# Kernel tuning notes

Measured on AMD Instinct MI355X. Metric: run time of the kernel, lower is better.

Reference implementation:

```python
import jax, jax.numpy as jnp
import numpy as np

POSE_IDS = np.array([0, 4, 8, 12, 16])
BN_EPS = 1e-5


def setup_inputs() -> dict:
    key = jax.random.key(0)
    ks = jax.random.split(key, 8)
    N, C, H, W = 64, 2048, 24, 12
    P, Cl = 5, 256
    Cm = C + P * Cl  # 3328
    return {
        "x": jax.random.normal(ks[0], (N, C, H, W), jnp.float32),
        "poses": jax.random.uniform(ks[1], (N, 17, 4), jnp.float32),
        "local_w": jax.random.normal(ks[2], (P, Cl, C), jnp.float32) * 0.02,
        "local_b": jnp.zeros((P, Cl), jnp.float32),
        "local_gamma": jnp.ones((P, Cl), jnp.float32),
        "local_beta": jnp.zeros((P, Cl), jnp.float32),
        "local_mean": jax.random.normal(ks[3], (P, Cl), jnp.float32) * 0.1,
        "local_var": jax.random.uniform(ks[4], (P, Cl), jnp.float32, 0.5, 1.5),
        "merge_w": jax.random.normal(ks[5], (C, Cm), jnp.float32) * 0.02,
        "merge_b": jnp.zeros((C,), jnp.float32),
        "merge_gamma": jnp.ones((C,), jnp.float32),
        "merge_beta": jnp.zeros((C,), jnp.float32),
        "merge_mean": jax.random.normal(ks[6], (C,), jnp.float32) * 0.1,
        "merge_var": jax.random.uniform(ks[7], (C,), jnp.float32, 0.5, 1.5),
    }


def reference(x, poses, local_w, local_b, local_gamma, local_beta, local_mean,
              local_var, merge_w, merge_b, merge_gamma, merge_beta, merge_mean,
              merge_var):
    N, C, H, W = x.shape
    kp = poses[:, jnp.asarray(POSE_IDS), :]  # [N,P,4]
    # box = [left, top, w, h]; clamp to [0, 0.75]; scale whole box by confidence
    half = jnp.full_like(kp[..., 0], 0.5)
    box = jnp.stack([kp[..., 0] - 0.25, kp[..., 1] - 0.25, half, half], axis=-1)
    box = jnp.clip(box, 0.0, 0.75) * kp[..., 2:3]
    # integer ROI bounds on the feature grid (round-half-to-even like torch)
    xs = jnp.maximum(0, jnp.round(W * box[..., 0])).astype(jnp.int32)          # [N,P]
    xe = jnp.minimum(W - 1, jnp.round(W * (box[..., 0] + box[..., 2]))).astype(jnp.int32)
    ys = jnp.maximum(0, jnp.round(H * box[..., 1])).astype(jnp.int32)
    ye = jnp.minimum(H - 1, jnp.round(H * (box[..., 1] + box[..., 3]))).astype(jnp.int32)
    rows = jnp.arange(H)
    cols = jnp.arange(W)
    mh = (rows[None, None, :] >= ys[..., None]) & (rows[None, None, :] < ye[..., None])  # [N,P,H]
    mw = (cols[None, None, :] >= xs[..., None]) & (cols[None, None, :] < xe[..., None])  # [N,P,W]
    mask = (mh[..., :, None] & mw[..., None, :]).astype(x.dtype)  # [N,P,H,W]
    # masked average pool over the ROI (single pass over x)
    sums = jnp.einsum('nchw,nphw->npc', x, mask)
    area = ((ye - ys) * (xe - xs)).astype(x.dtype)
    avg = sums / jnp.where(area > 0, area, 1.0)[..., None]  # [N,P,C], 0 for empty ROIs
    # per-part 1x1 conv + BN(eval) + ReLU -> [N,P,Cl]
    loc = jnp.einsum('npc,pkc->npk', avg, local_w) + local_b[None]
    loc = (loc - local_mean[None]) * (local_gamma[None] / jnp.sqrt(local_var[None] + BN_EPS)) + local_beta[None]
    loc = jax.nn.relu(loc)
    # global max pool -> [N,C]
    gfeat = x.max(axis=(2, 3))
    cat = jnp.concatenate([loc.reshape(N, -1), gfeat], axis=1)  # [N, P*Cl + C]
    # merge 1x1 conv + BN(eval) + ReLU
    y = cat @ merge_w.T + merge_b
    y = (y - merge_mean) * (merge_gamma / jnp.sqrt(merge_var + BN_EPS)) + merge_beta
    y = jax.nn.relu(y)
    # F.normalize(p=2, dim=1)
    norm = jnp.linalg.norm(y, axis=1, keepdims=True)
    return y / jnp.maximum(norm, 1e-12)
```

## Files before the change

### kernel.cpp

```cpp
#include <hip/hip_runtime.h>

#define N_   64
#define C_   2048
#define HW_  288
#define P_   5
#define CM_  3328
#define LOC_ 1280
#define SEGC 8
#define SEGM 13

#define PITCH 28

__global__ __launch_bounds__(256) void kB(const float* __restrict__ x,
    const float* __restrict__ poses,
    float* __restrict__ avg, float* __restrict__ cat) {
  __shared__ float lds[2][256 * PITCH];
  const int t  = threadIdx.x;
  const int n  = blockIdx.x >> 3;
  const int cb = (blockIdx.x & 7) << 8;
  const int chbase = n * C_ + cb;

  unsigned MH[P_], MW[P_];
  float INV[P_];
  const float* kpn = poses + (size_t)n * 68;
#pragma unroll
  for (int p = 0; p < P_; ++p) {
    const float* kp = kpn + 16 * p;
    float px = kp[0], py = kp[1], z = kp[2];
    float bx = fminf(fmaxf(px - 0.25f, 0.f), 0.75f) * z;
    float by = fminf(fmaxf(py - 0.25f, 0.f), 0.75f) * z;
    float bw = 0.5f * z;
    float bh = 0.5f * z;
    int xs = (int)fmaxf(0.f,  rintf(12.f * bx));
    int xe = (int)fminf(11.f, rintf(12.f * (bx + bw)));
    int ys = (int)fmaxf(0.f,  rintf(24.f * by));
    int ye = (int)fminf(23.f, rintf(24.f * (by + bh)));
    MH[p] = ((1u << ye) - 1u) & ~((1u << ys) - 1u);
    MW[p] = ((1u << xe) - 1u) & ~((1u << xs) - 1u);
    int area = (ye - ys) * (xe - xs);
    INV[p] = area > 0 ? 1.f / (float)area : 1.f;
  }

  const float4* x4 = (const float4*)x;
  size_t gbase[6];
  int    loff[6];
#pragma unroll
  for (int k = 0; k < 6; ++k) {
    unsigned flat = k * 256 + t;
    unsigned cl = flat / 6u;
    unsigned j  = flat - 6u * cl;
    gbase[k] = (size_t)(chbase + cl) * 72 + j;
    loff[k]  = cl * PITCH + 4 * j;
  }

  float4 rg[6];
  auto loadRegs = [&](int ci) {
#pragma unroll
    for (int k = 0; k < 6; ++k) rg[k] = x4[gbase[k] + ci * 6];
  };
  auto writeRegs = [&](int db) {
#pragma unroll
    for (int k = 0; k < 6; ++k) *(float4*)&lds[db][loff[k]] = rg[k];
  };

  float s[P_] = {0.f, 0.f, 0.f, 0.f, 0.f};
  float mx = -3.402823466e+38f;

  loadRegs(0);
  writeRegs(0);
  __syncthreads();
  for (int ci = 0; ci < 12; ++ci) {
    if (ci + 1 < 12) loadRegs(ci + 1);
    const float* row = &lds[ci & 1][t * PITCH];
#pragma unroll
    for (int r = 0; r < 2; ++r) {
      int h = 2 * ci + r;
      float4 a = *(const float4*)(row + r * 12 + 0);
      float4 b = *(const float4*)(row + r * 12 + 4);
      float4 c = *(const float4*)(row + r * 12 + 8);
      float m1 = fmaxf(fmaxf(a.x, a.y), fmaxf(a.z, a.w));
      float m2 = fmaxf(fmaxf(b.x, b.y), fmaxf(b.z, b.w));
      float m3 = fmaxf(fmaxf(c.x, c.y), fmaxf(c.z, c.w));
      mx = fmaxf(mx, fmaxf(m1, fmaxf(m2, m3)));
#pragma unroll
      for (int p = 0; p < P_; ++p) {
        unsigned cm = ((MH[p] >> h) & 1u) ? MW[p] : 0u;
        if (cm) {
          float t0 = ((cm & 0x001u) ? a.x : 0.f) + ((cm & 0x002u) ? a.y : 0.f);
          float t1 = ((cm & 0x004u) ? a.z : 0.f) + ((cm & 0x008u) ? a.w : 0.f);
          float t2 = ((cm & 0x010u) ? b.x : 0.f) + ((cm & 0x020u) ? b.y : 0.f);
          float t3 = ((cm & 0x040u) ? b.z : 0.f) + ((cm & 0x080u) ? b.w : 0.f);
          float t4 = ((cm & 0x100u) ? c.x : 0.f) + ((cm & 0x200u) ? c.y : 0.f);
          float t5 = ((cm & 0x400u) ? c.z : 0.f) + ((cm & 0x800u) ? c.w : 0.f);
          s[p] += ((t0 + t1) + (t2 + t3)) + (t4 + t5);
        }
      }
    }
    if (ci + 1 < 12) {
      writeRegs((ci + 1) & 1);
      __syncthreads();
    }
  }

  int c = cb + t;
  cat[(size_t)n * CM_ + LOC_ + c] = mx;
#pragma unroll
  for (int p = 0; p < P_; ++p)
    avg[((size_t)n * P_ + p) * C_ + c] = s[p] * INV[p];
}

template<int GSEG>
__device__ __forceinline__ void gemm_tile(const float* __restrict__ Ag, int lda,
                                          const float* __restrict__ Wg, int ldw,
                                          float* __restrict__ Og, int ldo,
                                          float* As, float* Ws) {
  const int t  = threadIdx.x;
  const int nq = t & 15;
  const int kq = t >> 4;
  const int c4 = (t & 15) << 2;
  const int rr = t >> 4;
  float acc[4][4] = {};
  for (int g = 0; g < GSEG; ++g) {
    __syncthreads();
#pragma unroll
    for (int i = 0; i < 4; ++i) {
      int r = rr + (i << 4);
      *(float4*)&As[r * 68 + c4] = *(const float4*)&Ag[(size_t)r * lda + (g << 6) + c4];
      *(float4*)&Ws[r * 68 + c4] = *(const float4*)&Wg[(size_t)r * ldw + (g << 6) + c4];
    }
    __syncthreads();
#pragma unroll
    for (int c = 0; c < 64; c += 4) {
      float4 a[4], w[4];
#pragma unroll
      for (int i = 0; i < 4; ++i) a[i] = *(const float4*)&As[(nq + (i << 4)) * 68 + c];
#pragma unroll
      for (int j = 0; j < 4; ++j) w[j] = *(const float4*)&Ws[(kq + (j << 4)) * 68 + c];
#pragma unroll
      for (int i = 0; i < 4; ++i)
#pragma unroll
        for (int j = 0; j < 4; ++j)
          acc[i][j] += a[i].x * w[j].x + a[i].y * w[j].y + a[i].z * w[j].z + a[i].w * w[j].w;
    }
  }
#pragma unroll
  for (int i = 0; i < 4; ++i)
#pragma unroll
    for (int j = 0; j < 4; ++j)
      Og[(size_t)(nq + (i << 4)) * ldo + kq + (j << 4)] = acc[i][j];
}

__global__ __launch_bounds__(256) void kC(const float* __restrict__ avg,
                                          const float* __restrict__ local_w,
                                          float* __restrict__ locP) {
  __shared__ float As[64 * 68];
  __shared__ float Ws[64 * 68];
  int b  = blockIdx.x;
  int tl = b >> 3;
  int sg = b & 7;
  int p  = tl >> 2;
  int kt = tl & 3;
  const float* Ag = avg + p * C_ + (sg << 8);
  const float* Wg = local_w + ((size_t)p * 256 + (kt << 6)) * C_ + (sg << 8);
  float* Og = locP + (size_t)sg * (N_ * LOC_) + (p << 8) + (kt << 6);
  gemm_tile<4>(Ag, P_ * C_, Wg, C_, Og, LOC_, As, Ws);
}

__global__ __launch_bounds__(256) void kC2(const float* __restrict__ locP,
    const float* __restrict__ lb, const float* __restrict__ lg, const float* __restrict__ lbe,
    const float* __restrict__ lm, const float* __restrict__ lv,
    float* __restrict__ cat) {
  int i = blockIdx.x * 256 + threadIdx.x;
  int n = i / LOC_;
  int q = i - n * LOC_;
  float s = 0.f;
#pragma unroll
  for (int sg = 0; sg < SEGC; ++sg) s += locP[(size_t)sg * (N_ * LOC_) + i];
  float sc = lg[q] / sqrtf(lv[q] + 1e-5f);
  float v = (s + lb[q] - lm[q]) * sc + lbe[q];
  cat[(size_t)n * CM_ + q] = fmaxf(v, 0.f);
}

__global__ __launch_bounds__(256) void kD(const float* __restrict__ cat,
                                          const float* __restrict__ merge_w,
                                          float* __restrict__ mrgP) {
  __shared__ float As[64 * 68];
  __shared__ float Ws[64 * 68];
  int b  = blockIdx.x;
  int jt = b / SEGM;
  int sg = b - jt * SEGM;
  const float* Ag = cat + (sg << 8);
  const float* Wg = merge_w + (size_t)(jt << 6) * CM_ + (sg << 8);
  float* Og = mrgP + (size_t)sg * (N_ * C_) + (jt << 6);
  gemm_tile<4>(Ag, CM_, Wg, CM_, Og, C_, As, Ws);
}

__global__ __launch_bounds__(256) void kE(const float* __restrict__ mrgP,
    const float* __restrict__ mb, const float* __restrict__ mg, const float* __restrict__ mbe,
    const float* __restrict__ mm, const float* __restrict__ mv,
    float* __restrict__ out) {
  int n = blockIdx.x, t = threadIdx.x;
  float z[8]; float ss = 0.f;
#pragma unroll
  for (int r = 0; r < 8; ++r) {
    int j = t + (r << 8);
    float y = 0.f;
#pragma unroll
    for (int sg = 0; sg < SEGM; ++sg) y += mrgP[(size_t)sg * (N_ * C_) + (size_t)n * C_ + j];
    float sc = mg[j] / sqrtf(mv[j] + 1e-5f);
    float v = (y + mb[j] - mm[j]) * sc + mbe[j];
    v = fmaxf(v, 0.f);
    z[r] = v; ss += v * v;
  }
#pragma unroll
  for (int off = 32; off; off >>= 1) ss += __shfl_xor(ss, off, 64);
  __shared__ float red[4];
  if ((t & 63) == 0) red[t >> 6] = ss;
  __syncthreads();
  float tot = red[0] + red[1] + red[2] + red[3];
  float inv = 1.f / fmaxf(sqrtf(tot), 1e-12f);
#pragma unroll
  for (int r = 0; r < 8; ++r) out[(size_t)n * C_ + t + (r << 8)] = z[r] * inv;
}

extern "C" void kernel_launch(void* const* d_in, const int* in_sizes, int n_in,
                              void* d_out, int out_size, void* d_ws, size_t ws_size,
                              hipStream_t stream) {
  const float* x          = (const float*)d_in[0];
  const float* poses      = (const float*)d_in[1];
  const float* local_w    = (const float*)d_in[2];
  const float* local_b    = (const float*)d_in[3];
  const float* local_g    = (const float*)d_in[4];
  const float* local_be   = (const float*)d_in[5];
  const float* local_m    = (const float*)d_in[6];
  const float* local_v    = (const float*)d_in[7];
  const float* merge_w    = (const float*)d_in[8];
  const float* merge_b    = (const float*)d_in[9];
  const float* merge_g    = (const float*)d_in[10];
  const float* merge_be   = (const float*)d_in[11];
  const float* merge_m    = (const float*)d_in[12];
  const float* merge_v    = (const float*)d_in[13];

  float* ws   = (float*)d_ws;
  float* cat  = ws;
  float* avg  = ws + 212992;
  float* locP = ws + 868352;
  float* mrgP = ws + 1523712;

  kB<<<512, 256, 0, stream>>>(x, poses, avg, cat);
  kC<<<20 * SEGC, 256, 0, stream>>>(avg, local_w, locP);
  kC2<<<(N_ * LOC_) / 256, 256, 0, stream>>>(locP, local_b, local_g, local_be,
                                             local_m, local_v, cat);
  kD<<<32 * SEGM, 256, 0, stream>>>(cat, merge_w, mrgP);
  kE<<<N_, 256, 0, stream>>>(mrgP, merge_b, merge_g, merge_be, merge_m, merge_v,
                             (float*)d_out);
}
```

Measured before the change: 335.2 us.

## Use bf16 MFMA for local and merge GEMMs with bf16 activation buffers

```diff
diff --git a/kernel.cpp b/kernel.cpp
--- a/kernel.cpp
+++ b/kernel.cpp
@@ -9,11 +9,24 @@
 #define SEGC 8
 #define SEGM 13
 
-#define PITCH 28
+#define PITCH  28
+#define WPITCH 72
+
+typedef __attribute__((ext_vector_type(8))) short bf16x8;
+typedef __attribute__((ext_vector_type(4))) float f32x4;
+
+__device__ __forceinline__ unsigned short f2bf(float f) {
+  unsigned u = __float_as_uint(f);
+  u = (u + 0x7FFFu + ((u >> 16) & 1u)) >> 16;
+  return (unsigned short)u;
+}
+__device__ __forceinline__ unsigned pack2(float lo, float hi) {
+  return (unsigned)f2bf(lo) | ((unsigned)f2bf(hi) << 16);
+}
 
 __global__ __launch_bounds__(256) void kB(const float* __restrict__ x,
     const float* __restrict__ poses,
-    float* __restrict__ avg, float* __restrict__ cat) {
+    unsigned short* __restrict__ avgB, unsigned short* __restrict__ catB) {
   __shared__ float lds[2][256 * PITCH];
   const int t  = threadIdx.x;
   const int n  = blockIdx.x >> 3;
@@ -103,73 +116,78 @@
   }
 
   int c = cb + t;
-  cat[(size_t)n * CM_ + LOC_ + c] = mx;
+  catB[(size_t)n * CM_ + LOC_ + c] = f2bf(mx);
 #pragma unroll
   for (int p = 0; p < P_; ++p)
-    avg[((size_t)n * P_ + p) * C_ + c] = s[p] * INV[p];
-}
-
-template<int GSEG>
-__device__ __forceinline__ void gemm_tile(const float* __restrict__ Ag, int lda,
-                                          const float* __restrict__ Wg, int ldw,
-                                          float* __restrict__ Og, int ldo,
-                                          float* As, float* Ws) {
+    avgB[((size_t)n * 5 + p) * C_ + c] = f2bf(s[p] * INV[p]);
+}
+
+__device__ __forceinline__ void mfma_seg(const uint4* __restrict__ aRow,
+                                         const float4* __restrict__ wRow,
+                                         unsigned short* As, unsigned short* Ws,
+                                         f32x4 acc[4]) {
   const int t  = threadIdx.x;
-  const int nq = t & 15;
-  const int kq = t >> 4;
-  const int c4 = (t & 15) << 2;
-  const int rr = t >> 4;
-  float acc[4][4] = {};
-  for (int g = 0; g < GSEG; ++g) {
+  const int kq = t & 3;
+  const int row = t >> 2;
+  const int w  = t >> 6;
+  const int l  = t & 63;
+  unsigned short* aw = &As[row * WPITCH + kq * 16];
+  unsigned short* ww = &Ws[row * WPITCH + kq * 16];
+  const int arow16 = (16 * w + (l & 15)) * WPITCH + (l >> 4) * 8;
+  const int brow16 = (l & 15) * WPITCH + (l >> 4) * 8;
+  for (int g = 0; g < 4; ++g) {
+    uint4 a0 = aRow[g * 8 + 0], a1 = aRow[g * 8 + 1];
+    float4 w0 = wRow[g * 16 + 0], w1 = wRow[g * 16 + 1],
+           w2 = wRow[g * 16 + 2], w3 = wRow[g * 16 + 3];
+    uint4 pw0, pw1;
+    pw0.x = pack2(w0.x, w0.y); pw0.y = pack2(w0.z, w0.w);
+    pw0.z = pack2(w1.x, w1.y); pw0.w = pack2(w1.z, w1.w);
+    pw1.x = pack2(w2.x, w2.y); pw1.y = pack2(w2.z, w2.w);
+    pw1.z = pack2(w3.x, w3.y); pw1.w = pack2(w3.z, w3.w);
+    if (g) __syncthreads();
+    *(uint4*)aw = a0; *(uint4*)(aw + 8) = a1;
+    *(uint4*)ww = pw0; *(uint4*)(ww + 8) = pw1;
     __syncthreads();
 #pragma unroll
-    for (int i = 0; i < 4; ++i) {
-      int r = rr + (i << 4);
-      *(float4*)&As[r * 68 + c4] = *(const float4*)&Ag[(size_t)r * lda + (g << 6) + c4];
-      *(float4*)&Ws[r * 68 + c4] = *(const float4*)&Wg[(size_t)r * ldw + (g << 6) + c4];
+    for (int s = 0; s < 2; ++s) {
+      bf16x8 af = *(const bf16x8*)&As[arow16 + s * 32];
+#pragma unroll
+      for (int jm = 0; jm < 4; ++jm) {
+        bf16x8 bf = *(const bf16x8*)&Ws[jm * 16 * WPITCH + brow16 + s * 32];
+        acc[jm] = __builtin_amdgcn_mfma_f32_16x16x32_bf16(af, bf, acc[jm], 0, 0, 0);
+      }
     }
-    __syncthreads();
-#pragma unroll
-    for (int c = 0; c < 64; c += 4) {
-      float4 a[4], w[4];
-#pragma unroll
-      for (int i = 0; i < 4; ++i) a[i] = *(const float4*)&As[(nq + (i << 4)) * 68 + c];
-#pragma unroll
-      for (int j = 0; j < 4; ++j) w[j] = *(const float4*)&Ws[(kq + (j << 4)) * 68 + c];
-#pragma unroll
-      for (int i = 0; i < 4; ++i)
-#pragma unroll
-        for (int j = 0; j < 4; ++j)
-          acc[i][j] += a[i].x * w[j].x + a[i].y * w[j].y + a[i].z * w[j].z + a[i].w * w[j].w;
-    }
-  }
-#pragma unroll
-  for (int i = 0; i < 4; ++i)
-#pragma unroll
-    for (int j = 0; j < 4; ++j)
-      Og[(size_t)(nq + (i << 4)) * ldo + kq + (j << 4)] = acc[i][j];
-}
-
-__global__ __launch_bounds__(256) void kC(const float* __restrict__ avg,
+  }
+}
+
+__global__ __launch_bounds__(256) void kC(const unsigned short* __restrict__ avgB,
                                           const float* __restrict__ local_w,
                                           float* __restrict__ locP) {
-  __shared__ float As[64 * 68];
-  __shared__ float Ws[64 * 68];
+  __shared__ unsigned short As[64 * WPITCH];
+  __shared__ unsigned short Ws[64 * WPITCH];
   int b  = blockIdx.x;
-  int tl = b >> 3;
+  int p  = b >> 5;
+  int kt = (b >> 3) & 3;
   int sg = b & 7;
-  int p  = tl >> 2;
-  int kt = tl & 3;
-  const float* Ag = avg + p * C_ + (sg << 8);
-  const float* Wg = local_w + ((size_t)p * 256 + (kt << 6)) * C_ + (sg << 8);
-  float* Og = locP + (size_t)sg * (N_ * LOC_) + (p << 8) + (kt << 6);
-  gemm_tile<4>(Ag, P_ * C_, Wg, C_, Og, LOC_, As, Ws);
+  const int t = threadIdx.x, row = t >> 2, kq = t & 3, w = t >> 6, l = t & 63;
+  const uint4*  aRow = (const uint4*)avgB + ((size_t)row * 5 + p) * 256 + sg * 32 + kq * 2;
+  const float4* wRow = (const float4*)(local_w + ((size_t)p * 256 + kt * 64 + row) * C_
+                                       + sg * 256 + kq * 16);
+  f32x4 acc[4] = {{0,0,0,0},{0,0,0,0},{0,0,0,0},{0,0,0,0}};
+  mfma_seg(aRow, wRow, As, Ws, acc);
+  float* outp = locP + (size_t)sg * (N_ * LOC_);
+#pragma unroll
+  for (int jm = 0; jm < 4; ++jm)
+#pragma unroll
+    for (int r = 0; r < 4; ++r)
+      outp[(size_t)(16 * w + (l >> 4) * 4 + r) * LOC_ + p * 256 + kt * 64 + jm * 16 + (l & 15)]
+        = acc[jm][r];
 }
 
 __global__ __launch_bounds__(256) void kC2(const float* __restrict__ locP,
     const float* __restrict__ lb, const float* __restrict__ lg, const float* __restrict__ lbe,
     const float* __restrict__ lm, const float* __restrict__ lv,
-    float* __restrict__ cat) {
+    unsigned short* __restrict__ catB) {
   int i = blockIdx.x * 256 + threadIdx.x;
   int n = i / LOC_;
   int q = i - n * LOC_;
@@ -178,21 +196,30 @@
   for (int sg = 0; sg < SEGC; ++sg) s += locP[(size_t)sg * (N_ * LOC_) + i];
   float sc = lg[q] / sqrtf(lv[q] + 1e-5f);
   float v = (s + lb[q] - lm[q]) * sc + lbe[q];
-  cat[(size_t)n * CM_ + q] = fmaxf(v, 0.f);
-}
-
-__global__ __launch_bounds__(256) void kD(const float* __restrict__ cat,
+  catB[(size_t)n * CM_ + q] = f2bf(fmaxf(v, 0.f));
+}
+
+__global__ __launch_bounds__(256) void kD(const unsigned short* __restrict__ catB,
                                           const float* __restrict__ merge_w,
                                           float* __restrict__ mrgP) {
-  __shared__ float As[64 * 68];
-  __shared__ float Ws[64 * 68];
+  __shared__ unsigned short As[64 * WPITCH];
+  __shared__ unsigned short Ws[64 * WPITCH];
   int b  = blockIdx.x;
   int jt = b / SEGM;
   int sg = b - jt * SEGM;
-  const float* Ag = cat + (sg << 8);
-  const float* Wg = merge_w + (size_t)(jt << 6) * CM_ + (sg << 8);
-  float* Og = mrgP + (size_t)sg * (N_ * C_) + (jt << 6);
-  gemm_tile<4>(Ag, CM_, Wg, CM_, Og, C_, As, Ws);
+  const int t = threadIdx.x, row = t >> 2, kq = t & 3, w = t >> 6, l = t & 63;
+  const uint4*  aRow = (const uint4*)catB + (size_t)row * 416 + sg * 32 + kq * 2;
+  const float4* wRow = (const float4*)(merge_w + (size_t)(jt * 64 + row) * CM_
+                                       + sg * 256 + kq * 16);
+  f32x4 acc[4] = {{0,0,0,0},{0,0,0,0},{0,0,0,0},{0,0,0,0}};
+  mfma_seg(aRow, wRow, As, Ws, acc);
+  float* outp = mrgP + (size_t)sg * (N_ * C_);
+#pragma unroll
+  for (int jm = 0; jm < 4; ++jm)
+#pragma unroll
+    for (int r = 0; r < 4; ++r)
+      outp[(size_t)(16 * w + (l >> 4) * 4 + r) * C_ + jt * 64 + jm * 16 + (l & 15)]
+        = acc[jm][r];
 }
 
 __global__ __launch_bounds__(256) void kE(const float* __restrict__ mrgP,
@@ -241,17 +268,17 @@
   const float* merge_m    = (const float*)d_in[12];
   const float* merge_v    = (const float*)d_in[13];
 
-  float* ws   = (float*)d_ws;
-  float* cat  = ws;
-  float* avg  = ws + 212992;
-  float* locP = ws + 868352;
-  float* mrgP = ws + 1523712;
-
-  kB<<<512, 256, 0, stream>>>(x, poses, avg, cat);
-  kC<<<20 * SEGC, 256, 0, stream>>>(avg, local_w, locP);
+  char* ws = (char*)d_ws;
+  unsigned short* catB = (unsigned short*)ws;
+  unsigned short* avgB = (unsigned short*)(ws + 425984);
+  float* locP = (float*)(ws + 1736704);
+  float* mrgP = (float*)(ws + 4358144);
+
+  kB<<<512, 256, 0, stream>>>(x, poses, avgB, catB);
+  kC<<<20 * SEGC, 256, 0, stream>>>(avgB, local_w, locP);
   kC2<<<(N_ * LOC_) / 256, 256, 0, stream>>>(locP, local_b, local_g, local_be,
-                                             local_m, local_v, cat);
-  kD<<<32 * SEGM, 256, 0, stream>>>(cat, merge_w, mrgP);
+                                             local_m, local_v, catB);
+  kD<<<32 * SEGM, 256, 0, stream>>>(catB, merge_w, mrgP);
   kE<<<N_, 256, 0, stream>>>(mrgP, merge_b, merge_g, merge_be, merge_m, merge_v,
                              (float*)d_out);
 }
```

New measurement: 294.7 us. 12.1% less time.
